# Kernel tuning notes

Measured on AMD Instinct MI355X. Metric: run time of the kernel, lower is better.

Reference implementation:

```python
import jax, jax.numpy as jnp
import numpy as np

N_NODES = 100000
N_EDGES = 1600000
N_GRAPHS = 512
IN_CH = 128
HID_CH = 128   # 2 * out_channels
OUT_CH = 64


def gcn_conv(x, edge_index, W, b, num_nodes):
    """PyG GCNConv: x' = D^-1/2 (A+I) D^-1/2 (x W) + b (symmetric norm, self loops)."""
    h = x @ W  # [N, F_out]
    loops = jnp.arange(num_nodes, dtype=edge_index.dtype)
    src = jnp.concatenate([edge_index[0], loops])  # j (source)
    dst = jnp.concatenate([edge_index[1], loops])  # i (target)
    deg = jax.ops.segment_sum(jnp.ones_like(dst, dtype=h.dtype), dst,
                              num_segments=num_nodes)  # in-degree incl. self loop
    dinv = jnp.where(deg > 0, jax.lax.rsqrt(deg), 0.0)
    norm = dinv[src] * dinv[dst]  # [E+N]
    msgs = h[src] * norm[:, None]  # gather + scale, [E+N, F_out]
    out = jax.ops.segment_sum(msgs, dst, num_segments=num_nodes)
    return out + b


def global_mean_pool(x, batch, num_graphs):
    sums = jax.ops.segment_sum(x, batch, num_segments=num_graphs)
    cnts = jax.ops.segment_sum(jnp.ones((x.shape[0],), x.dtype), batch,
                               num_segments=num_graphs)
    return sums / jnp.maximum(cnts, 1.0)[:, None]


def setup_inputs() -> dict:
    key = jax.random.key(0)
    k = jax.random.split(key, 6)
    x = jax.random.normal(k[0], (N_NODES, IN_CH), dtype=jnp.float32)
    edge_index = jax.random.randint(k[1], (2, N_EDGES), 0, N_NODES, dtype=jnp.int64)
    batch = jnp.sort(jax.random.randint(k[2], (N_NODES,), 0, N_GRAPHS, dtype=jnp.int64))
    W1 = jax.random.normal(k[3], (IN_CH, HID_CH), dtype=jnp.float32) * (1.0 / np.sqrt(IN_CH))
    b1 = jnp.zeros((HID_CH,), dtype=jnp.float32)
    W2 = jax.random.normal(k[4], (HID_CH, OUT_CH), dtype=jnp.float32) * (1.0 / np.sqrt(HID_CH))
    b2 = jnp.zeros((OUT_CH,), dtype=jnp.float32)
    return {"x": x, "edge_index": edge_index, "batch": batch,
            "W1": W1, "b1": b1, "W2": W2, "b2": b2}


def reference(x, edge_index, batch, W1, b1, W2, b2):
    h = gcn_conv(x, edge_index, W1, b1, N_NODES)
    h = jax.nn.relu(h)
    h = gcn_conv(h, edge_index, W2, b2, N_NODES)
    return global_mean_pool(h, batch, N_GRAPHS)  # [num_graphs, out_channels]
```

## Files before the change

kernel.cpp:

```cpp
#include <hip/hip_runtime.h>
#include <hip/hip_fp16.h>

#define NN 100000
#define NE 1600000
#define NG 512
#define NBLK 391
#define EPB 8192
#define NCB 196
#define EPBS 4096
#define NCBS 391

typedef _Float16 half8 __attribute__((ext_vector_type(8)));
typedef _Float16 half4v __attribute__((ext_vector_type(4)));
typedef float floatx4 __attribute__((ext_vector_type(4)));

__global__ __launch_bounds__(256) void k_bhist(const int* __restrict__ dst,
                                               int* __restrict__ bcnt) {
    __shared__ int h[NBLK];
    int t = threadIdx.x;
    for (int i = t; i < NBLK; i += 256) h[i] = 0;
    __syncthreads();
    int e0 = blockIdx.x * EPB;
    int e1 = e0 + EPB; if (e1 > NE) e1 = NE;
    for (int i = e0 + t; i < e1; i += 256) atomicAdd(&h[dst[i] >> 8], 1);
    __syncthreads();
    for (int i = t; i < NBLK; i += 256)
        if (h[i]) atomicAdd(&bcnt[i], h[i]);
}

__global__ __launch_bounds__(512) void k_bscan(const int* __restrict__ bcnt,
                                               int* __restrict__ bbase,
                                               int* __restrict__ gcur) {
    __shared__ int s[512];
    int t = threadIdx.x;
    int v = (t < NBLK) ? bcnt[t] : 0;
    s[t] = v;
    __syncthreads();
    for (int d = 1; d < 512; d <<= 1) {
        int u = (t >= d) ? s[t - d] : 0;
        __syncthreads();
        s[t] += u;
        __syncthreads();
    }
    if (t < NBLK) {
        int ex = s[t] - v;
        bbase[t] = ex;
        gcur[t] = ex;
    }
    if (t == 0) bbase[NBLK] = NE;
}

__global__ __launch_bounds__(256) void k_csort(const int* __restrict__ src,
                                               const int* __restrict__ dst,
                                               int* __restrict__ gcur,
                                               unsigned* __restrict__ pairbuf) {
    __shared__ int hcnt[NBLK];
    __shared__ int lbase[NBLK];
    __shared__ int lcur[NBLK];
    __shared__ int gbase[NBLK];
    __shared__ int ss[512];
    __shared__ unsigned sorted[EPBS];
    __shared__ unsigned short bkt[EPBS];
    int t = threadIdx.x;
    int e0 = blockIdx.x * EPBS;
    int e1 = e0 + EPBS; if (e1 > NE) e1 = NE;
    int n = e1 - e0;

    for (int i = t; i < NBLK; i += 256) hcnt[i] = 0;
    __syncthreads();
    for (int i = e0 + t; i < e1; i += 256)
        atomicAdd(&hcnt[dst[i] >> 8], 1);
    __syncthreads();
    ss[t]       = (t < NBLK) ? hcnt[t] : 0;
    ss[t + 256] = (t + 256 < NBLK) ? hcnt[t + 256] : 0;
    __syncthreads();
    for (int d = 1; d < 512; d <<= 1) {
        int v1 = (t >= d) ? ss[t - d] : 0;
        int v2 = ss[t + 256 - d];
        __syncthreads();
        ss[t] += v1; ss[t + 256] += v2;
        __syncthreads();
    }
    for (int i = t; i < NBLK; i += 256) {
        int ex = ss[i] - hcnt[i];
        lbase[i] = ex;
        lcur[i] = ex;
        if (hcnt[i] > 0) gbase[i] = atomicAdd(&gcur[i], hcnt[i]);
    }
    __syncthreads();
    for (int i = e0 + t; i < e1; i += 256) {
        int d = dst[i];
        int b = d >> 8;
        int pos = atomicAdd(&lcur[b], 1);
        sorted[pos] = ((unsigned)(d & 255) << 24) | (unsigned)src[i];
        bkt[pos] = (unsigned short)b;
    }
    __syncthreads();
    for (int i = t; i < n; i += 256) {
        int b = bkt[i];
        pairbuf[gbase[b] + (i - lbase[b])] = sorted[i];
    }
}

__global__ __launch_bounds__(256) void k_offs_place(
    const unsigned* __restrict__ pairbuf, const int* __restrict__ bbase,
    int* __restrict__ offs, float* __restrict__ dinv, int* __restrict__ csr) {
    __shared__ int dcnt[256];
    __shared__ int p[256];
    __shared__ int lcur[256];
    int t = threadIdx.x;
    int b = blockIdx.x;
    int base = bbase[b];
    int cnt = bbase[b + 1] - base;
    int node0 = b << 8;
    dcnt[t] = 0;
    __syncthreads();
    for (int i = t; i < cnt; i += 256)
        atomicAdd(&dcnt[pairbuf[base + i] >> 24], 1);
    __syncthreads();
    int v = dcnt[t];
    p[t] = v;
    __syncthreads();
    for (int d = 1; d < 256; d <<= 1) {
        int u = (t >= d) ? p[t - d] : 0;
        __syncthreads();
        p[t] += u;
        __syncthreads();
    }
    int ex = p[t] - v;
    lcur[t] = ex;
    int node = node0 + t;
    if (node <= NN) offs[node] = base + ex;
    if (node < NN) dinv[node] = rsqrtf((float)(v + 1));
    __syncthreads();
    for (int i = t; i < cnt; i += 256) {
        unsigned e = pairbuf[base + i];
        int slot = atomicAdd(&lcur[e >> 24], 1);
        csr[base + slot] = (int)(e & 0xFFFFFFu);
    }
}

__global__ void k_wt(const float* __restrict__ W, __half* __restrict__ Wt, int fout) {
    int idx = blockIdx.x * 256 + threadIdx.x;
    if (idx < 128 * fout) {
        int k = idx / fout, n = idx % fout;
        Wt[n * 128 + k] = __float2half(W[idx]);
    }
}

template <int FOUT, bool HALF_IN>
__global__ __launch_bounds__(256) void k_mm_mfma(const void* __restrict__ Xv,
                                                 const __half* __restrict__ Wt,
                                                 const float* __restrict__ dinv,
                                                 __half* __restrict__ Out) {
    constexpr int PITCH = 136;
    __shared__ _Float16 Xs[64 * PITCH];
    __shared__ _Float16 Ws[FOUT * PITCH];
    int t = threadIdx.x;
    int row0 = blockIdx.x * 64;

    if (HALF_IN) {
        const __half* X = (const __half*)Xv;
        for (int i = t; i < 64 * 16; i += 256) {
            int r = i >> 4, kg = i & 15;
            int row = row0 + r;
            half8 v = {};
            if (row < NN) v = *(const half8*)(X + (size_t)row * 128 + kg * 8);
            *(half8*)(Xs + r * PITCH + kg * 8) = v;
        }
    } else {
        const float* X = (const float*)Xv;
        for (int i = t; i < 64 * 32; i += 256) {
            int r = i >> 5, f4 = i & 31;
            int row = row0 + r;
            half4v h = {};
            if (row < NN) {
                float4 v = *(const float4*)(X + (size_t)row * 128 + f4 * 4);
                h[0] = (_Float16)v.x; h[1] = (_Float16)v.y;
                h[2] = (_Float16)v.z; h[3] = (_Float16)v.w;
            }
            *(half4v*)(Xs + r * PITCH + f4 * 4) = h;
        }
    }
    for (int i = t; i < FOUT * 16; i += 256) {
        int n = i >> 4, kg = i & 15;
        *(half8*)(Ws + n * PITCH + kg * 8) = *(const half8*)(Wt + n * 128 + kg * 8);
    }
    __syncthreads();

    int wave = t >> 6, lane = t & 63;
    int m = lane & 15, quad = lane >> 4;
    int wrow = wave * 16;
    constexpr int NCT = FOUT / 16;
    floatx4 acc[NCT];
#pragma unroll
    for (int c = 0; c < NCT; ++c) acc[c] = (floatx4){0.f, 0.f, 0.f, 0.f};

#pragma unroll
    for (int kc = 0; kc < 4; ++kc) {
        half8 a = *(const half8*)(Xs + (wrow + m) * PITCH + kc * 32 + quad * 8);
#pragma unroll
        for (int c = 0; c < NCT; ++c) {
            half8 b = *(const half8*)(Ws + (c * 16 + m) * PITCH + kc * 32 + quad * 8);
            acc[c] = __builtin_amdgcn_mfma_f32_16x16x32_f16(a, b, acc[c], 0, 0, 0);
        }
    }

    float dv[4];
    int rowb = row0 + wrow + quad * 4;
#pragma unroll
    for (int r = 0; r < 4; ++r) dv[r] = (rowb + r < NN) ? dinv[rowb + r] : 0.f;
#pragma unroll
    for (int c = 0; c < NCT; ++c) {
#pragma unroll
        for (int r = 0; r < 4; ++r) {
            int row = rowb + r;
            if (row < NN)
                Out[(size_t)row * FOUT + c * 16 + m] = __float2half(acc[c][r] * dv[r]);
        }
    }
}

__global__ __launch_bounds__(256) void k_agg_mm(
    const __half* __restrict__ G, const int* __restrict__ csr,
    const int* __restrict__ offs, const float* __restrict__ dinv,
    const float* __restrict__ bias1, const __half* __restrict__ Wt2,
    __half* __restrict__ G2) {
    constexpr int PITCH = 136;
    __shared__ _Float16 Brows[16 * PITCH];
    __shared__ _Float16 Ws[64 * PITCH];
    int t = threadIdx.x;
    for (int i = t; i < 64 * 16; i += 256) {
        int n = i >> 4, kg = i & 15;
        *(half8*)(Ws + n * PITCH + kg * 8) = *(const half8*)(Wt2 + n * 128 + kg * 8);
    }
    int wave = t >> 6, lane = t & 63;
    int sub = lane >> 4, fl = lane & 15;
    int ni = wave * 4 + sub;
    int node = blockIdx.x * 16 + ni;
    const _Float16* g = (const _Float16*)G;
    float acc[8];
    {
        half8 v = *(const half8*)(g + (size_t)node * 128 + fl * 8);
#pragma unroll
        for (int j = 0; j < 8; ++j) acc[j] = (float)v[j];
    }
    int e0 = offs[node], e1 = offs[node + 1];
    int e = e0;
    for (; e + 8 <= e1; e += 8) {
        int s0 = csr[e],     s1 = csr[e + 1], s2 = csr[e + 2], s3 = csr[e + 3];
        int s4 = csr[e + 4], s5 = csr[e + 5], s6 = csr[e + 6], s7 = csr[e + 7];
        half8 v0 = *(const half8*)(g + (size_t)s0 * 128 + fl * 8);
        half8 v1 = *(const half8*)(g + (size_t)s1 * 128 + fl * 8);
        half8 v2 = *(const half8*)(g + (size_t)s2 * 128 + fl * 8);
        half8 v3 = *(const half8*)(g + (size_t)s3 * 128 + fl * 8);
        half8 v4 = *(const half8*)(g + (size_t)s4 * 128 + fl * 8);
        half8 v5 = *(const half8*)(g + (size_t)s5 * 128 + fl * 8);
        half8 v6 = *(const half8*)(g + (size_t)s6 * 128 + fl * 8);
        half8 v7 = *(const half8*)(g + (size_t)s7 * 128 + fl * 8);
#pragma unroll
        for (int j = 0; j < 8; ++j)
            acc[j] += (((float)v0[j] + (float)v1[j]) + ((float)v2[j] + (float)v3[j])) +
                      (((float)v4[j] + (float)v5[j]) + ((float)v6[j] + (float)v7[j]));
    }
    for (; e + 4 <= e1; e += 4) {
        int s0 = csr[e], s1 = csr[e + 1], s2 = csr[e + 2], s3 = csr[e + 3];
        half8 v0 = *(const half8*)(g + (size_t)s0 * 128 + fl * 8);
        half8 v1 = *(const half8*)(g + (size_t)s1 * 128 + fl * 8);
        half8 v2 = *(const half8*)(g + (size_t)s2 * 128 + fl * 8);
        half8 v3 = *(const half8*)(g + (size_t)s3 * 128 + fl * 8);
#pragma unroll
        for (int j = 0; j < 8; ++j)
            acc[j] += ((float)v0[j] + (float)v1[j]) + ((float)v2[j] + (float)v3[j]);
    }
    for (; e < e1; ++e) {
        half8 v = *(const half8*)(g + (size_t)csr[e] * 128 + fl * 8);
#pragma unroll
        for (int j = 0; j < 8; ++j) acc[j] += (float)v[j];
    }
    {
        float di = dinv[node];
        float4 b0 = *(const float4*)(bias1 + fl * 8);
        float4 b1 = *(const float4*)(bias1 + fl * 8 + 4);
        half8 h;
        h[0] = (_Float16)fmaxf(acc[0] * di + b0.x, 0.f);
        h[1] = (_Float16)fmaxf(acc[1] * di + b0.y, 0.f);
        h[2] = (_Float16)fmaxf(acc[2] * di + b0.z, 0.f);
        h[3] = (_Float16)fmaxf(acc[3] * di + b0.w, 0.f);
        h[4] = (_Float16)fmaxf(acc[4] * di + b1.x, 0.f);
        h[5] = (_Float16)fmaxf(acc[5] * di + b1.y, 0.f);
        h[6] = (_Float16)fmaxf(acc[6] * di + b1.z, 0.f);
        h[7] = (_Float16)fmaxf(acc[7] * di + b1.w, 0.f);
        *(half8*)(Brows + ni * PITCH + fl * 8) = h;
    }
    __syncthreads();
    int m = lane & 15, quad = lane >> 4;
    floatx4 c = (floatx4){0.f, 0.f, 0.f, 0.f};
#pragma unroll
    for (int kc = 0; kc < 4; ++kc) {
        half8 a = *(const half8*)(Brows + m * PITCH + kc * 32 + quad * 8);
        half8 b = *(const half8*)(Ws + (wave * 16 + m) * PITCH + kc * 32 + quad * 8);
        c = __builtin_amdgcn_mfma_f32_16x16x32_f16(a, b, c, 0, 0, 0);
    }
    int rowb = blockIdx.x * 16 + quad * 4;
#pragma unroll
    for (int r = 0; r < 4; ++r) {
        float dv = dinv[rowb + r];
        G2[(size_t)(rowb + r) * 64 + wave * 16 + m] = __float2half(c[r] * dv);
    }
}

__global__ __launch_bounds__(256) void k_agg_pool(
    const __half* __restrict__ G, const int* __restrict__ csr,
    const int* __restrict__ offs, const float* __restrict__ dinv,
    const int* __restrict__ batch, float* __restrict__ gsum) {
    __shared__ float bsum[4][64];
    int t = threadIdx.x;
    int wave = t >> 6, lane = t & 63;
    int sub = lane >> 3, fl = lane & 7;
    int n0 = blockIdx.x * 32;
    int nb = n0 + wave * 8;
    int node = nb + sub;
    const _Float16* g = (const _Float16*)G;
    float acc[8];
    {
        half8 v = *(const half8*)(g + (size_t)node * 64 + fl * 8);
#pragma unroll
        for (int j = 0; j < 8; ++j) acc[j] = (float)v[j];
    }
    int e0 = offs[node], e1 = offs[node + 1];
    int e = e0;
    for (; e + 8 <= e1; e += 8) {
        int s0 = csr[e],     s1 = csr[e + 1], s2 = csr[e + 2], s3 = csr[e + 3];
        int s4 = csr[e + 4], s5 = csr[e + 5], s6 = csr[e + 6], s7 = csr[e + 7];
        half8 v0 = *(const half8*)(g + (size_t)s0 * 64 + fl * 8);
        half8 v1 = *(const half8*)(g + (size_t)s1 * 64 + fl * 8);
        half8 v2 = *(const half8*)(g + (size_t)s2 * 64 + fl * 8);
        half8 v3 = *(const half8*)(g + (size_t)s3 * 64 + fl * 8);
        half8 v4 = *(const half8*)(g + (size_t)s4 * 64 + fl * 8);
        half8 v5 = *(const half8*)(g + (size_t)s5 * 64 + fl * 8);
        half8 v6 = *(const half8*)(g + (size_t)s6 * 64 + fl * 8);
        half8 v7 = *(const half8*)(g + (size_t)s7 * 64 + fl * 8);
#pragma unroll
        for (int j = 0; j < 8; ++j)
            acc[j] += (((float)v0[j] + (float)v1[j]) + ((float)v2[j] + (float)v3[j])) +
                      (((float)v4[j] + (float)v5[j]) + ((float)v6[j] + (float)v7[j]));
    }
    for (; e + 4 <= e1; e += 4) {
        int s0 = csr[e], s1 = csr[e + 1], s2 = csr[e + 2], s3 = csr[e + 3];
        half8 v0 = *(const half8*)(g + (size_t)s0 * 64 + fl * 8);
        half8 v1 = *(const half8*)(g + (size_t)s1 * 64 + fl * 8);
        half8 v2 = *(const half8*)(g + (size_t)s2 * 64 + fl * 8);
        half8 v3 = *(const half8*)(g + (size_t)s3 * 64 + fl * 8);
#pragma unroll
        for (int j = 0; j < 8; ++j)
            acc[j] += ((float)v0[j] + (float)v1[j]) + ((float)v2[j] + (float)v3[j]);
    }
    for (; e < e1; ++e) {
        half8 v = *(const half8*)(g + (size_t)csr[e] * 64 + fl * 8);
#pragma unroll
        for (int j = 0; j < 8; ++j) acc[j] += (float)v[j];
    }
    float di = dinv[node];
#pragma unroll
    for (int j = 0; j < 8; ++j) acc[j] *= di;

    bool buni = (batch[n0] == batch[n0 + 31]);
    if (buni) {
#pragma unroll
        for (int j = 0; j < 8; ++j) {
            float s = acc[j];
            s += __shfl_xor(s, 8);
            s += __shfl_xor(s, 16);
            s += __shfl_xor(s, 32);
            acc[j] = s;
        }
        if (sub == 0) {
#pragma unroll
            for (int j = 0; j < 8; ++j) bsum[wave][fl * 8 + j] = acc[j];
        }
        __syncthreads();
        if (t < 64) {
            float tot = (bsum[0][t] + bsum[1][t]) + (bsum[2][t] + bsum[3][t]);
            atomicAdd(&gsum[batch[n0] * 64 + t], tot);
        }
    } else {
        int gph = batch[node];
        bool uni = (batch[nb] == batch[nb + 7]);
        if (uni) {
#pragma unroll
            for (int j = 0; j < 8; ++j) {
                float s = acc[j];
                s += __shfl_xor(s, 8);
                s += __shfl_xor(s, 16);
                s += __shfl_xor(s, 32);
                acc[j] = s;
            }
            if (sub == 0) {
#pragma unroll
                for (int j = 0; j < 8; ++j)
                    atomicAdd(&gsum[gph * 64 + fl * 8 + j], acc[j]);
            }
        } else {
#pragma unroll
            for (int j = 0; j < 8; ++j)
                atomicAdd(&gsum[gph * 64 + fl * 8 + j], acc[j]);
        }
    }
}

__global__ __launch_bounds__(64) void k_pool2(const float* __restrict__ gsum,
                                              const int* __restrict__ batch,
                                              const float* __restrict__ b2,
                                              float* __restrict__ out) {
    int gph = blockIdx.x;
    int f = threadIdx.x;
    int lo = 0, hi = NN;
    while (lo < hi) { int m = (lo + hi) >> 1; if (batch[m] < gph) lo = m + 1; else hi = m; }
    int s0 = lo;
    hi = NN;
    while (lo < hi) { int m = (lo + hi) >> 1; if (batch[m] <= gph) lo = m + 1; else hi = m; }
    int cnt = lo - s0;
    out[gph * 64 + f] = (cnt > 0) ? gsum[gph * 64 + f] / (float)cnt + b2[f] : 0.f;
}

extern "C" void kernel_launch(void* const* d_in, const int* in_sizes, int n_in,
                              void* d_out, int out_size, void* d_ws, size_t ws_size,
                              hipStream_t stream) {
    const float* x     = (const float*)d_in[0];
    const int*   ei    = (const int*)d_in[1];
    const int*   batch = (const int*)d_in[2];
    const float* W1    = (const float*)d_in[3];
    const float* b1    = (const float*)d_in[4];
    const float* W2    = (const float*)d_in[5];
    const float* b2    = (const float*)d_in[6];
    const int* esrc = ei;
    const int* edst = ei + NE;

    char* ws = (char*)d_ws;
    size_t off = 0;
    __half* G1  = (__half*)(ws + off); off += (size_t)NN * 128 * 2;
    __half* G2  = (__half*)(ws + off); off += (size_t)NN * 64 * 2;
    float* gsum = (float*)(ws + off);  off += (size_t)NG * 64 * 4;
    int*   csr  = (int*)(ws + off);    off += (size_t)NE * 4;
    unsigned* pairbuf = (unsigned*)(ws + off); off += (size_t)NE * 4;
    int*   offs = (int*)(ws + off);    off += ((size_t)NN + 8) * 4;
    float* dinv = (float*)(ws + off);  off += (size_t)NN * 4;
    int*   bcnt = (int*)(ws + off);    off += 512 * 4;
    int*   bbase= (int*)(ws + off);    off += 512 * 4;
    int*   gcur = (int*)(ws + off);    off += 512 * 4;
    __half* Wt1 = (__half*)(ws + off); off += 128 * 128 * 2;
    __half* Wt2 = (__half*)(ws + off); off += 128 * 64 * 2;

    hipMemsetAsync(bcnt, 0, 512 * sizeof(int), stream);
    hipMemsetAsync(gsum, 0, (size_t)NG * 64 * sizeof(float), stream);
    k_bhist<<<NCB, 256, 0, stream>>>(edst, bcnt);
    k_bscan<<<1, 512, 0, stream>>>(bcnt, bbase, gcur);
    k_csort<<<NCBS, 256, 0, stream>>>(esrc, edst, gcur, pairbuf);
    k_offs_place<<<NBLK, 256, 0, stream>>>(pairbuf, bbase, offs, dinv, csr);

    k_wt<<<64, 256, 0, stream>>>(W1, Wt1, 128);
    k_wt<<<32, 256, 0, stream>>>(W2, Wt2, 64);

    const int MMB = (NN + 63) / 64;
    k_mm_mfma<128, false><<<MMB, 256, 0, stream>>>(x, Wt1, dinv, G1);
    k_agg_mm<<<NN / 16, 256, 0, stream>>>(G1, csr, offs, dinv, b1, Wt2, G2);
    k_agg_pool<<<NN / 32, 256, 0, stream>>>(G2, csr, offs, dinv, batch, gsum);
    k_pool2<<<NG, 64, 0, stream>>>(gsum, batch, b2, (float*)d_out);
}
```

Before: 308.3 us.

## Split each node's edge list across lane groups in the aggregation kernels

Both aggregation kernels now loop over 8 nodes per wave, and each node's incoming edges are strided across lane sub-groups (4 groups in agg_mm, 8 in agg_pool), followed by a shuffle reduction. Previously each sub-group handled one node's whole edge list. The goal is to balance the irregular degrees across lanes and to raise memory-level parallelism in the gather. In agg_mm each block now covers 32 nodes and issues two MFMAs per k-step, halving the block count and reusing the Ws staging. The two weight-transpose launches are merged into one. The cost is a serial per-node loop per wave with shuffle-reduction overhead, and pooling accumulates per wave before any atomics.

```diff
diff --git a/kernel.cpp b/kernel.cpp
--- a/kernel.cpp
+++ b/kernel.cpp
@@ -140,11 +140,18 @@
     }
 }
 
-__global__ void k_wt(const float* __restrict__ W, __half* __restrict__ Wt, int fout) {
+__global__ void k_wtboth(const float* __restrict__ W1, const float* __restrict__ W2,
+                         __half* __restrict__ Wt1, __half* __restrict__ Wt2) {
     int idx = blockIdx.x * 256 + threadIdx.x;
-    if (idx < 128 * fout) {
-        int k = idx / fout, n = idx % fout;
-        Wt[n * 128 + k] = __float2half(W[idx]);
+    if (idx < 128 * 128) {
+        int k = idx >> 7, n = idx & 127;
+        Wt1[n * 128 + k] = __float2half(W1[idx]);
+    } else {
+        int j = idx - 128 * 128;
+        if (j < 128 * 64) {
+            int k = j / 64, n = j % 64;
+            Wt2[n * 128 + k] = __float2half(W2[j]);
+        }
     }
 }
 
@@ -227,7 +234,7 @@
     const float* __restrict__ bias1, const __half* __restrict__ Wt2,
     __half* __restrict__ G2) {
     constexpr int PITCH = 136;
-    __shared__ _Float16 Brows[16 * PITCH];
+    __shared__ _Float16 Brows[32 * PITCH];
     __shared__ _Float16 Ws[64 * PITCH];
     int t = threadIdx.x;
     for (int i = t; i < 64 * 16; i += 256) {
@@ -236,77 +243,84 @@
     }
     int wave = t >> 6, lane = t & 63;
     int sub = lane >> 4, fl = lane & 15;
-    int ni = wave * 4 + sub;
-    int node = blockIdx.x * 16 + ni;
     const _Float16* g = (const _Float16*)G;
-    float acc[8];
-    {
-        half8 v = *(const half8*)(g + (size_t)node * 128 + fl * 8);
-#pragma unroll
-        for (int j = 0; j < 8; ++j) acc[j] = (float)v[j];
-    }
-    int e0 = offs[node], e1 = offs[node + 1];
-    int e = e0;
-    for (; e + 8 <= e1; e += 8) {
-        int s0 = csr[e],     s1 = csr[e + 1], s2 = csr[e + 2], s3 = csr[e + 3];
-        int s4 = csr[e + 4], s5 = csr[e + 5], s6 = csr[e + 6], s7 = csr[e + 7];
-        half8 v0 = *(const half8*)(g + (size_t)s0 * 128 + fl * 8);
-        half8 v1 = *(const half8*)(g + (size_t)s1 * 128 + fl * 8);
-        half8 v2 = *(const half8*)(g + (size_t)s2 * 128 + fl * 8);
-        half8 v3 = *(const half8*)(g + (size_t)s3 * 128 + fl * 8);
-        half8 v4 = *(const half8*)(g + (size_t)s4 * 128 + fl * 8);
-        half8 v5 = *(const half8*)(g + (size_t)s5 * 128 + fl * 8);
-        half8 v6 = *(const half8*)(g + (size_t)s6 * 128 + fl * 8);
-        half8 v7 = *(const half8*)(g + (size_t)s7 * 128 + fl * 8);
-#pragma unroll
-        for (int j = 0; j < 8; ++j)
-            acc[j] += (((float)v0[j] + (float)v1[j]) + ((float)v2[j] + (float)v3[j])) +
-                      (((float)v4[j] + (float)v5[j]) + ((float)v6[j] + (float)v7[j]));
-    }
-    for (; e + 4 <= e1; e += 4) {
-        int s0 = csr[e], s1 = csr[e + 1], s2 = csr[e + 2], s3 = csr[e + 3];
-        half8 v0 = *(const half8*)(g + (size_t)s0 * 128 + fl * 8);
-        half8 v1 = *(const half8*)(g + (size_t)s1 * 128 + fl * 8);
-        half8 v2 = *(const half8*)(g + (size_t)s2 * 128 + fl * 8);
-        half8 v3 = *(const half8*)(g + (size_t)s3 * 128 + fl * 8);
-#pragma unroll
-        for (int j = 0; j < 8; ++j)
-            acc[j] += ((float)v0[j] + (float)v1[j]) + ((float)v2[j] + (float)v3[j]);
-    }
-    for (; e < e1; ++e) {
-        half8 v = *(const half8*)(g + (size_t)csr[e] * 128 + fl * 8);
-#pragma unroll
-        for (int j = 0; j < 8; ++j) acc[j] += (float)v[j];
-    }
-    {
-        float di = dinv[node];
-        float4 b0 = *(const float4*)(bias1 + fl * 8);
-        float4 b1 = *(const float4*)(bias1 + fl * 8 + 4);
-        half8 h;
-        h[0] = (_Float16)fmaxf(acc[0] * di + b0.x, 0.f);
-        h[1] = (_Float16)fmaxf(acc[1] * di + b0.y, 0.f);
-        h[2] = (_Float16)fmaxf(acc[2] * di + b0.z, 0.f);
-        h[3] = (_Float16)fmaxf(acc[3] * di + b0.w, 0.f);
-        h[4] = (_Float16)fmaxf(acc[4] * di + b1.x, 0.f);
-        h[5] = (_Float16)fmaxf(acc[5] * di + b1.y, 0.f);
-        h[6] = (_Float16)fmaxf(acc[6] * di + b1.z, 0.f);
-        h[7] = (_Float16)fmaxf(acc[7] * di + b1.w, 0.f);
-        *(half8*)(Brows + ni * PITCH + fl * 8) = h;
+    int nbase = blockIdx.x * 32 + wave * 8;
+
+#pragma unroll 1
+    for (int i = 0; i < 8; ++i) {
+        int node = nbase + i;
+        float acc[8];
+        if (sub == 0) {
+            half8 v = *(const half8*)(g + (size_t)node * 128 + fl * 8);
+#pragma unroll
+            for (int j = 0; j < 8; ++j) acc[j] = (float)v[j];
+        } else {
+#pragma unroll
+            for (int j = 0; j < 8; ++j) acc[j] = 0.f;
+        }
+        int e0 = offs[node], e1 = offs[node + 1];
+        int e = e0 + sub;
+        for (; e + 12 < e1; e += 16) {
+            int s0 = csr[e], s1 = csr[e + 4], s2 = csr[e + 8], s3 = csr[e + 12];
+            half8 v0 = *(const half8*)(g + (size_t)s0 * 128 + fl * 8);
+            half8 v1 = *(const half8*)(g + (size_t)s1 * 128 + fl * 8);
+            half8 v2 = *(const half8*)(g + (size_t)s2 * 128 + fl * 8);
+            half8 v3 = *(const half8*)(g + (size_t)s3 * 128 + fl * 8);
+#pragma unroll
+            for (int j = 0; j < 8; ++j)
+                acc[j] += ((float)v0[j] + (float)v1[j]) + ((float)v2[j] + (float)v3[j]);
+        }
+        for (; e < e1; e += 4) {
+            half8 v = *(const half8*)(g + (size_t)csr[e] * 128 + fl * 8);
+#pragma unroll
+            for (int j = 0; j < 8; ++j) acc[j] += (float)v[j];
+        }
+#pragma unroll
+        for (int j = 0; j < 8; ++j) {
+            float s = acc[j];
+            s += __shfl_xor(s, 16);
+            s += __shfl_xor(s, 32);
+            acc[j] = s;
+        }
+        if (sub == 0) {
+            float di = dinv[node];
+            float4 b0 = *(const float4*)(bias1 + fl * 8);
+            float4 b1 = *(const float4*)(bias1 + fl * 8 + 4);
+            half8 h;
+            h[0] = (_Float16)fmaxf(acc[0] * di + b0.x, 0.f);
+            h[1] = (_Float16)fmaxf(acc[1] * di + b0.y, 0.f);
+            h[2] = (_Float16)fmaxf(acc[2] * di + b0.z, 0.f);
+            h[3] = (_Float16)fmaxf(acc[3] * di + b0.w, 0.f);
+            h[4] = (_Float16)fmaxf(acc[4] * di + b1.x, 0.f);
+            h[5] = (_Float16)fmaxf(acc[5] * di + b1.y, 0.f);
+            h[6] = (_Float16)fmaxf(acc[6] * di + b1.z, 0.f);
+            h[7] = (_Float16)fmaxf(acc[7] * di + b1.w, 0.f);
+            *(half8*)(Brows + (wave * 8 + i) * PITCH + fl * 8) = h;
+        }
     }
     __syncthreads();
     int m = lane & 15, quad = lane >> 4;
-    floatx4 c = (floatx4){0.f, 0.f, 0.f, 0.f};
+    floatx4 c0 = (floatx4){0.f, 0.f, 0.f, 0.f};
+    floatx4 c1 = (floatx4){0.f, 0.f, 0.f, 0.f};
 #pragma unroll
     for (int kc = 0; kc < 4; ++kc) {
-        half8 a = *(const half8*)(Brows + m * PITCH + kc * 32 + quad * 8);
         half8 b = *(const half8*)(Ws + (wave * 16 + m) * PITCH + kc * 32 + quad * 8);
-        c = __builtin_amdgcn_mfma_f32_16x16x32_f16(a, b, c, 0, 0, 0);
-    }
-    int rowb = blockIdx.x * 16 + quad * 4;
+        half8 a0 = *(const half8*)(Brows + m * PITCH + kc * 32 + quad * 8);
+        half8 a1 = *(const half8*)(Brows + (16 + m) * PITCH + kc * 32 + quad * 8);
+        c0 = __builtin_amdgcn_mfma_f32_16x16x32_f16(a0, b, c0, 0, 0, 0);
+        c1 = __builtin_amdgcn_mfma_f32_16x16x32_f16(a1, b, c1, 0, 0, 0);
+    }
+    int rowb = blockIdx.x * 32 + quad * 4;
 #pragma unroll
     for (int r = 0; r < 4; ++r) {
         float dv = dinv[rowb + r];
-        G2[(size_t)(rowb + r) * 64 + wave * 16 + m] = __float2half(c[r] * dv);
+        G2[(size_t)(rowb + r) * 64 + wave * 16 + m] = __float2half(c0[r] * dv);
+    }
+    rowb += 16;
+#pragma unroll
+    for (int r = 0; r < 4; ++r) {
+        float dv = dinv[rowb + r];
+        G2[(size_t)(rowb + r) * 64 + wave * 16 + m] = __float2half(c1[r] * dv);
     }
 }
 
@@ -319,54 +333,42 @@
     int wave = t >> 6, lane = t & 63;
     int sub = lane >> 3, fl = lane & 7;
     int n0 = blockIdx.x * 32;
-    int nb = n0 + wave * 8;
-    int node = nb + sub;
+    int nbase = n0 + wave * 8;
     const _Float16* g = (const _Float16*)G;
-    float acc[8];
-    {
-        half8 v = *(const half8*)(g + (size_t)node * 64 + fl * 8);
-#pragma unroll
-        for (int j = 0; j < 8; ++j) acc[j] = (float)v[j];
-    }
-    int e0 = offs[node], e1 = offs[node + 1];
-    int e = e0;
-    for (; e + 8 <= e1; e += 8) {
-        int s0 = csr[e],     s1 = csr[e + 1], s2 = csr[e + 2], s3 = csr[e + 3];
-        int s4 = csr[e + 4], s5 = csr[e + 5], s6 = csr[e + 6], s7 = csr[e + 7];
-        half8 v0 = *(const half8*)(g + (size_t)s0 * 64 + fl * 8);
-        half8 v1 = *(const half8*)(g + (size_t)s1 * 64 + fl * 8);
-        half8 v2 = *(const half8*)(g + (size_t)s2 * 64 + fl * 8);
-        half8 v3 = *(const half8*)(g + (size_t)s3 * 64 + fl * 8);
-        half8 v4 = *(const half8*)(g + (size_t)s4 * 64 + fl * 8);
-        half8 v5 = *(const half8*)(g + (size_t)s5 * 64 + fl * 8);
-        half8 v6 = *(const half8*)(g + (size_t)s6 * 64 + fl * 8);
-        half8 v7 = *(const half8*)(g + (size_t)s7 * 64 + fl * 8);
-#pragma unroll
-        for (int j = 0; j < 8; ++j)
-            acc[j] += (((float)v0[j] + (float)v1[j]) + ((float)v2[j] + (float)v3[j])) +
-                      (((float)v4[j] + (float)v5[j]) + ((float)v6[j] + (float)v7[j]));
-    }
-    for (; e + 4 <= e1; e += 4) {
-        int s0 = csr[e], s1 = csr[e + 1], s2 = csr[e + 2], s3 = csr[e + 3];
-        half8 v0 = *(const half8*)(g + (size_t)s0 * 64 + fl * 8);
-        half8 v1 = *(const half8*)(g + (size_t)s1 * 64 + fl * 8);
-        half8 v2 = *(const half8*)(g + (size_t)s2 * 64 + fl * 8);
-        half8 v3 = *(const half8*)(g + (size_t)s3 * 64 + fl * 8);
-#pragma unroll
-        for (int j = 0; j < 8; ++j)
-            acc[j] += ((float)v0[j] + (float)v1[j]) + ((float)v2[j] + (float)v3[j]);
-    }
-    for (; e < e1; ++e) {
-        half8 v = *(const half8*)(g + (size_t)csr[e] * 64 + fl * 8);
-#pragma unroll
-        for (int j = 0; j < 8; ++j) acc[j] += (float)v[j];
-    }
-    float di = dinv[node];
-#pragma unroll
-    for (int j = 0; j < 8; ++j) acc[j] *= di;
-
-    bool buni = (batch[n0] == batch[n0 + 31]);
-    if (buni) {
+    bool wuni = (batch[nbase] == batch[nbase + 7]);
+    float wacc[8];
+#pragma unroll
+    for (int j = 0; j < 8; ++j) wacc[j] = 0.f;
+
+#pragma unroll 1
+    for (int i = 0; i < 8; ++i) {
+        int node = nbase + i;
+        float acc[8];
+        if (sub == 0) {
+            half8 v = *(const half8*)(g + (size_t)node * 64 + fl * 8);
+#pragma unroll
+            for (int j = 0; j < 8; ++j) acc[j] = (float)v[j];
+        } else {
+#pragma unroll
+            for (int j = 0; j < 8; ++j) acc[j] = 0.f;
+        }
+        int e0 = offs[node], e1 = offs[node + 1];
+        int e = e0 + sub;
+        for (; e + 24 < e1; e += 32) {
+            int s0 = csr[e], s1 = csr[e + 8], s2 = csr[e + 16], s3 = csr[e + 24];
+            half8 v0 = *(const half8*)(g + (size_t)s0 * 64 + fl * 8);
+            half8 v1 = *(const half8*)(g + (size_t)s1 * 64 + fl * 8);
+            half8 v2 = *(const half8*)(g + (size_t)s2 * 64 + fl * 8);
+            half8 v3 = *(const half8*)(g + (size_t)s3 * 64 + fl * 8);
+#pragma unroll
+            for (int j = 0; j < 8; ++j)
+                acc[j] += ((float)v0[j] + (float)v1[j]) + ((float)v2[j] + (float)v3[j]);
+        }
+        for (; e < e1; e += 8) {
+            half8 v = *(const half8*)(g + (size_t)csr[e] * 64 + fl * 8);
+#pragma unroll
+            for (int j = 0; j < 8; ++j) acc[j] += (float)v[j];
+        }
 #pragma unroll
         for (int j = 0; j < 8; ++j) {
             float s = acc[j];
@@ -375,36 +377,39 @@
             s += __shfl_xor(s, 32);
             acc[j] = s;
         }
-        if (sub == 0) {
-#pragma unroll
-            for (int j = 0; j < 8; ++j) bsum[wave][fl * 8 + j] = acc[j];
+        float di = dinv[node];
+        if (wuni) {
+            if (sub == 0) {
+#pragma unroll
+                for (int j = 0; j < 8; ++j) wacc[j] += acc[j] * di;
+            }
+        } else {
+            if (sub == 0) {
+                int gph = batch[node];
+#pragma unroll
+                for (int j = 0; j < 8; ++j)
+                    atomicAdd(&gsum[gph * 64 + fl * 8 + j], acc[j] * di);
+            }
+        }
+    }
+
+    bool buni = (batch[n0] == batch[n0 + 31]);
+    if (buni) {
+        if (lane < 8) {
+#pragma unroll
+            for (int j = 0; j < 8; ++j) bsum[wave][lane * 8 + j] = wacc[j];
         }
         __syncthreads();
         if (t < 64) {
             float tot = (bsum[0][t] + bsum[1][t]) + (bsum[2][t] + bsum[3][t]);
             atomicAdd(&gsum[batch[n0] * 64 + t], tot);
         }
-    } else {
-        int gph = batch[node];
-        bool uni = (batch[nb] == batch[nb + 7]);
-        if (uni) {
-#pragma unroll
-            for (int j = 0; j < 8; ++j) {
-                float s = acc[j];
-                s += __shfl_xor(s, 8);
-                s += __shfl_xor(s, 16);
-                s += __shfl_xor(s, 32);
-                acc[j] = s;
-            }
-            if (sub == 0) {
-#pragma unroll
-                for (int j = 0; j < 8; ++j)
-                    atomicAdd(&gsum[gph * 64 + fl * 8 + j], acc[j]);
-            }
-        } else {
+    } else if (wuni) {
+        if (lane < 8) {
+            int gph = batch[nbase];
 #pragma unroll
             for (int j = 0; j < 8; ++j)
-                atomicAdd(&gsum[gph * 64 + fl * 8 + j], acc[j]);
+                atomicAdd(&gsum[gph * 64 + lane * 8 + j], wacc[j]);
         }
     }
 }
@@ -459,12 +464,11 @@
     k_csort<<<NCBS, 256, 0, stream>>>(esrc, edst, gcur, pairbuf);
     k_offs_place<<<NBLK, 256, 0, stream>>>(pairbuf, bbase, offs, dinv, csr);
 
-    k_wt<<<64, 256, 0, stream>>>(W1, Wt1, 128);
-    k_wt<<<32, 256, 0, stream>>>(W2, Wt2, 64);
+    k_wtboth<<<96, 256, 0, stream>>>(W1, W2, Wt1, Wt2);
 
     const int MMB = (NN + 63) / 64;
     k_mm_mfma<128, false><<<MMB, 256, 0, stream>>>(x, Wt1, dinv, G1);
-    k_agg_mm<<<NN / 16, 256, 0, stream>>>(G1, csr, offs, dinv, b1, Wt2, G2);
+    k_agg_mm<<<NN / 32, 256, 0, stream>>>(G1, csr, offs, dinv, b1, Wt2, G2);
     k_agg_pool<<<NN / 32, 256, 0, stream>>>(G2, csr, offs, dinv, batch, gsum);
     k_pool2<<<NG, 64, 0, stream>>>(gsum, batch, b2, (float*)d_out);
 }
```

Measured after the change: 353.0 us. 14.5% more time.
